# Kernel optimization log

Hardware: AMD Instinct MI355X
Metric: run time of the kernel (lower is better)

Reference implementation:

```python
import jax, jax.numpy as jnp
import numpy as np

B, L, D, H = 2, 1000, 288, 8
DIM = D // H          # 36 per-head dim
DFF = 2 * D           # 576 conv-FFN hidden
KS = L // 4           # 250 sampled keys per query
NQ = L // 4           # 250 selected (active) queries
EPS = 1e-5


def _layernorm(x, g, b):
    mu = x.mean(-1, keepdims=True)
    var = ((x - mu) ** 2).mean(-1, keepdims=True)
    return (x - mu) * jax.lax.rsqrt(var + EPS) * g + b


def _prob_attention(q, k, v, index_key):
    # q,k,v: [b,h,L,dim]; index_key: [L, KS]
    b, h, l, dim = q.shape
    # sample KS keys per query row (gather): [b,h,L,KS,dim]
    k_samp = jnp.take(k, index_key, axis=2)
    # sampled scores: [b,h,L,KS]
    scores_samp = jnp.einsum('bhld,bhlkd->bhlk', q, k_samp)
    # sparsity measure M(q) = max - mean(over full l_key, as in source)
    measure = scores_samp.max(-1) - scores_samp.sum(-1) / l
    # top-NQ active queries per (b,h): [b,h,NQ]
    idx_q = jax.lax.top_k(measure, NQ)[1]
    q_sel = jnp.take_along_axis(q, idx_q[..., None], axis=2)  # [b,h,NQ,dim]
    sim = jnp.einsum('bhqd,bhkd->bhqk', q_sel, k) * (1.0 / np.sqrt(dim))
    attn = jax.nn.softmax(sim, axis=-1)
    out_sel = jnp.einsum('bhqk,bhkd->bhqd', attn, v)          # [b,h,NQ,dim]
    # lazy queries get mean(V); scatter active outputs in
    out = jnp.broadcast_to(v.mean(axis=2, keepdims=True), v.shape)
    bi = jnp.arange(b)[:, None, None]
    hi = jnp.arange(h)[None, :, None]
    out = out.at[bi, hi, idx_q].set(out_sel)
    return out  # [b,h,L,dim]


def reference(x, index_key, Wq, bq, Wk, bk, Wv, bv, W1, b1, W2, b2,
              ln1_g, ln1_b, ln2_g, ln2_b):
    b, l, d = x.shape
    # QKV projections -> [b,h,L,dim]
    q = (x @ Wq.T + bq).reshape(b, l, H, DIM).transpose(0, 2, 1, 3)
    k = (x @ Wk.T + bk).reshape(b, l, H, DIM).transpose(0, 2, 1, 3)
    v = (x @ Wv.T + bv).reshape(b, l, H, DIM).transpose(0, 2, 1, 3)
    attn = _prob_attention(q, k, v, index_key)
    attn = attn.transpose(0, 2, 1, 3).reshape(b, l, d)
    # residual + LN1 (dropout is identity in eval)
    h1 = _layernorm(x + attn, ln1_g, ln1_b)
    # conv FFN (kernel_size=1 conv == per-position linear), exact GELU
    f = jax.nn.gelu(h1 @ W1.T + b1, approximate=False)   # [b,l,DFF]
    f = jax.nn.gelu(f @ W2.T + b2, approximate=False)    # [b,l,d]
    return _layernorm(f + h1, ln2_g, ln2_b)


def setup_inputs() -> dict:
    key = jax.random.key(0)
    ks = jax.random.split(key, 10)
    s = 0.05
    return {
        'x': jax.random.normal(ks[0], (B, L, D), jnp.float32),
        'index_key': jax.random.randint(ks[1], (L, KS), 0, L),
        'Wq': jax.random.normal(ks[2], (D, D), jnp.float32) * s,
        'bq': jnp.zeros((D,), jnp.float32),
        'Wk': jax.random.normal(ks[3], (D, D), jnp.float32) * s,
        'bk': jnp.zeros((D,), jnp.float32),
        'Wv': jax.random.normal(ks[4], (D, D), jnp.float32) * s,
        'bv': jnp.zeros((D,), jnp.float32),
        'W1': jax.random.normal(ks[5], (DFF, D), jnp.float32) * s,
        'b1': jnp.zeros((DFF,), jnp.float32),
        'W2': jax.random.normal(ks[6], (D, DFF), jnp.float32) * s,
        'b2': jnp.zeros((D,), jnp.float32),
        'ln1_g': jnp.ones((D,), jnp.float32),
        'ln1_b': jnp.zeros((D,), jnp.float32),
        'ln2_g': jnp.ones((D,), jnp.float32),
        'ln2_b': jnp.zeros((D,), jnp.float32),
    }
```

## Files before the change

kernel.cpp:

```cpp
#include <hip/hip_runtime.h>
#include <hip/hip_bf16.h>
#include <math.h>

#define B_ 2
#define L_ 1000
#define D_ 288
#define H_ 8
#define DIM_ 36
#define DFF_ 576
#define KS_ 250
#define NQ_ 250
#define BH_ (B_ * H_)
#define EPS_ 1e-5f
#define PSTRIDE_ 40

__device__ __forceinline__ float gelu_exact(float x) {
    return 0.5f * x * (1.0f + erff(x * 0.70710678118654752f));
}

__device__ __forceinline__ float dot4(float4 a, float4 b) {
    return a.x * b.x + a.y * b.y + a.z * b.z + a.w * b.w;
}

__global__ __launch_bounds__(256) void transpose_kernel(
    const float* __restrict__ src, float* __restrict__ dst,
    int Rr, int Cc, int ntx)
{
    __shared__ float tile[32][33];
    const int t = blockIdx.x;
    const int ty0 = (t / ntx) * 32, tx0 = (t % ntx) * 32;
    const int tx = threadIdx.x & 31, ty = threadIdx.x >> 5;
#pragma unroll
    for (int i = 0; i < 4; i++)
        tile[ty + 8 * i][tx] = src[(size_t)(ty0 + ty + 8 * i) * Cc + tx0 + tx];
    __syncthreads();
#pragma unroll
    for (int i = 0; i < 4; i++)
        dst[(size_t)(tx0 + ty + 8 * i) * Rr + ty0 + tx] = tile[tx][ty + 8 * i];
}

__global__ __launch_bounds__(256) void ktranspose_kernel(
    const float* __restrict__ K, float* __restrict__ KT)
{
    __shared__ float tile[32][33];
    const int t = blockIdx.x;
    const int bh = t >> 6;
    const int rem = t & 63;
    const int lt = rem >> 1, dt = rem & 1;
    const int l0 = lt * 32, d0 = dt * 32;
    const int tx = threadIdx.x & 31, ty = threadIdx.x >> 5;
    const float* Kb = K + (size_t)bh * L_ * DIM_;
    float* KTb = KT + (size_t)bh * DIM_ * L_;
#pragma unroll
    for (int i = 0; i < 4; i++) {
        int l = l0 + ty + 8 * i, d = d0 + tx;
        tile[ty + 8 * i][tx] = (l < L_ && d < DIM_) ? Kb[(size_t)l * DIM_ + d] : 0.f;
    }
    __syncthreads();
#pragma unroll
    for (int i = 0; i < 4; i++) {
        int d = d0 + ty + 8 * i, l = l0 + tx;
        if (d < DIM_ && l < L_) KTb[(size_t)d * L_ + l] = tile[tx][ty + 8 * i];
    }
}

__global__ __launch_bounds__(256) void qkvT2_kernel(
    const float* __restrict__ x,
    const float* __restrict__ WqT, const float* __restrict__ WkT,
    const float* __restrict__ WvT,
    const float* __restrict__ bq, const float* __restrict__ bk,
    const float* __restrict__ bv,
    float* __restrict__ Q, float* __restrict__ K, float* __restrict__ V)
{
    __shared__ float xsT[D_][4];
    const int base = blockIdx.x * 4;
    const int tid = threadIdx.x;

    for (int idx = tid; idx < 4 * D_; idx += 256) {
        int r = idx / D_, k = idx % D_;
        xsT[k][r] = x[(size_t)(base + r) * D_ + k];
    }
    __syncthreads();

    if (tid < 216) {
        const int gcol = 4 * tid;
        const int m = gcol / D_;
        const int c = gcol - m * D_;
        const float* WT = (m == 0) ? WqT : (m == 1) ? WkT : WvT;
        const float* bias = (m == 0) ? bq : (m == 1) ? bk : bv;
        float* outp = (m == 0) ? Q : (m == 1) ? K : V;

        float a[4][4];
#pragma unroll
        for (int j = 0; j < 4; j++) {
            float bv2 = bias[c + j];
#pragma unroll
            for (int r = 0; r < 4; r++) a[j][r] = bv2;
        }

        for (int k = 0; k < D_; k++) {
            float4 w = *(const float4*)(WT + (size_t)k * D_ + c);
            float4 xv = *(const float4*)&xsT[k][0];
            a[0][0] += w.x * xv.x; a[0][1] += w.x * xv.y; a[0][2] += w.x * xv.z; a[0][3] += w.x * xv.w;
            a[1][0] += w.y * xv.x; a[1][1] += w.y * xv.y; a[1][2] += w.y * xv.z; a[1][3] += w.y * xv.w;
            a[2][0] += w.z * xv.x; a[2][1] += w.z * xv.y; a[2][2] += w.z * xv.z; a[2][3] += w.z * xv.w;
            a[3][0] += w.w * xv.x; a[3][1] += w.w * xv.y; a[3][2] += w.w * xv.z; a[3][3] += w.w * xv.w;
        }

#pragma unroll
        for (int j = 0; j < 4; j++) {
            int col = c + j;
            int h = col / DIM_, dd = col % DIM_;
#pragma unroll
            for (int r = 0; r < 4; r++) {
                int row = base + r;
                int b = row / L_, l = row % L_;
                outp[((size_t)(b * H_ + h) * L_ + l) * DIM_ + dd] = a[j][r];
            }
        }
    }
}

__global__ __launch_bounds__(320) void qkv_kernel(
    const float* __restrict__ x,
    const float* __restrict__ Wq, const float* __restrict__ bq,
    const float* __restrict__ Wk, const float* __restrict__ bk,
    const float* __restrict__ Wv, const float* __restrict__ bv,
    float* __restrict__ Q, float* __restrict__ K, float* __restrict__ V)
{
    constexpr int R = 8;
    __shared__ float xs[R][D_];
    const int base = blockIdx.x * R;
    const int tid = threadIdx.x;

    const float4* xsrc = (const float4*)(x + (size_t)base * D_);
    float4* xdst = (float4*)&xs[0][0];
    for (int i = tid; i < R * D_ / 4; i += 320) xdst[i] = xsrc[i];
    __syncthreads();

    if (tid < D_) {
        const float4* wq4 = (const float4*)(Wq + (size_t)tid * D_);
        const float4* wk4 = (const float4*)(Wk + (size_t)tid * D_);
        const float4* wv4 = (const float4*)(Wv + (size_t)tid * D_);
        float aq[R], ak[R], av[R];
        float biasq = bq[tid], biask = bk[tid], biasv = bv[tid];
#pragma unroll
        for (int r = 0; r < R; r++) { aq[r] = biasq; ak[r] = biask; av[r] = biasv; }
        for (int d4 = 0; d4 < D_ / 4; d4++) {
            float4 wqv = wq4[d4], wkv = wk4[d4], wvv = wv4[d4];
#pragma unroll
            for (int r = 0; r < R; r++) {
                float4 hv = *(const float4*)&xs[r][d4 * 4];
                aq[r] += dot4(hv, wqv);
                ak[r] += dot4(hv, wkv);
                av[r] += dot4(hv, wvv);
            }
        }
        const int h = tid / DIM_, dd = tid % DIM_;
#pragma unroll
        for (int r = 0; r < R; r++) {
            int row = base + r;
            int b = row / L_, l = row % L_;
            size_t o = ((size_t)(b * H_ + h) * L_ + l) * DIM_ + dd;
            Q[o] = aq[r]; K[o] = ak[r]; V[o] = av[r];
        }
    }
}

__global__ __launch_bounds__(256) void vmean_kernel(
    const float* __restrict__ V, float* __restrict__ Vmean)
{
    const int bh = blockIdx.x;
    const int tid = threadIdx.x;
    __shared__ float red[7][DIM_];
    if (tid < 252) {
        int g = tid / DIM_, d = tid % DIM_;
        const float* base = V + (size_t)bh * L_ * DIM_;
        float s = 0.f;
        for (int l = g; l < L_; l += 7) s += base[l * DIM_ + d];
        red[g][d] = s;
    }
    __syncthreads();
    if (tid < DIM_) {
        float s = 0.f;
#pragma unroll
        for (int g = 0; g < 7; g++) s += red[g][tid];
        Vmean[bh * DIM_ + tid] = s * (1.0f / L_);
    }
}

__global__ __launch_bounds__(256) void score_measure3_kernel(
    const float* __restrict__ Q, const float* __restrict__ KT,
    const int* __restrict__ index_key, float* __restrict__ measure)
{
    constexpr int R = 8;
    __shared__ float qs[R][DIM_];
    __shared__ float st[R][1004];
    const int bh = blockIdx.x / 125;
    const int qt = blockIdx.x % 125;
    const int tid = threadIdx.x;

    if (tid < R * DIM_ / 4)
        ((float4*)&qs[0][0])[tid] =
            ((const float4*)(Q + ((size_t)bh * L_ + qt * R) * DIM_))[tid];
    __syncthreads();

    const float* KTb = KT + (size_t)bh * DIM_ * L_;
#pragma unroll
    for (int i = 0; i < 4; i++) {
        const int k = i * 256 + tid;
        if (k < L_) {
            float acc[R];
#pragma unroll
            for (int r = 0; r < R; r++) acc[r] = 0.f;
#pragma unroll
            for (int d4 = 0; d4 < DIM_ / 4; d4++) {
                float4 kv;
                kv.x = KTb[(size_t)(d4 * 4 + 0) * L_ + k];
                kv.y = KTb[(size_t)(d4 * 4 + 1) * L_ + k];
                kv.z = KTb[(size_t)(d4 * 4 + 2) * L_ + k];
                kv.w = KTb[(size_t)(d4 * 4 + 3) * L_ + k];
#pragma unroll
                for (int r = 0; r < R; r++)
                    acc[r] += dot4(*(const float4*)&qs[r][d4 * 4], kv);
            }
#pragma unroll
            for (int r = 0; r < R; r++) st[r][k] = acc[r];
        }
    }
    __syncthreads();

    const int r = tid >> 5;
    const int lane = tid & 31;
    const int l = qt * R + r;
    const int* ik = index_key + l * KS_;
    float mx = -1e30f, sm = 0.f;
    for (int s = lane; s < KS_; s += 32) {
        float v = st[r][ik[s]];
        mx = fmaxf(mx, v);
        sm += v;
    }
#pragma unroll
    for (int off = 16; off; off >>= 1) {
        mx = fmaxf(mx, __shfl_xor(mx, off));
        sm += __shfl_xor(sm, off);
    }
    if (lane == 0) measure[bh * L_ + l] = mx - sm * (1.0f / (float)L_);
}

__global__ __launch_bounds__(256) void measure_kernel(
    const float* __restrict__ Q, const float* __restrict__ K,
    const int* __restrict__ index_key, float* __restrict__ measure)
{
    const int w = threadIdx.x >> 6;
    const int lane = threadIdx.x & 63;
    const int wid = blockIdx.x * 4 + w;
    const int bh = wid / L_;
    const int l = wid % L_;

    const float4* qp = (const float4*)(Q + ((size_t)bh * L_ + l) * DIM_);
    float4 q[9];
#pragma unroll
    for (int i = 0; i < 9; i++) q[i] = qp[i];

    const int* ik = index_key + l * KS_;
    const float* Kb = K + (size_t)bh * L_ * DIM_;

    float mx = -1e30f, sm = 0.f;
#pragma unroll
    for (int s = lane; s < KS_; s += 64) {
        int kidx = ik[s];
        const float4* k4 = (const float4*)(Kb + (size_t)kidx * DIM_);
        float acc = 0.f;
#pragma unroll
        for (int i = 0; i < 9; i++) acc += dot4(q[i], k4[i]);
        mx = fmaxf(mx, acc);
        sm += acc;
    }
#pragma unroll
    for (int off = 32; off; off >>= 1) {
        mx = fmaxf(mx, __shfl_xor(mx, off));
        sm += __shfl_xor(sm, off);
    }
    if (lane == 0) measure[wid] = mx - sm * (1.0f / (float)L_);
}

__global__ __launch_bounds__(256) void topk_kernel(
    const float* __restrict__ measure, int* __restrict__ qlist,
    int* __restrict__ qcnt)
{
    const int bh = blockIdx.x >> 2;
    const int quarter = blockIdx.x & 3;
    __shared__ float m[L_];
    for (int i = threadIdx.x; i < L_; i += 256) m[i] = measure[bh * L_ + i];
    __syncthreads();
    const int i = quarter * 250 + threadIdx.x;
    if (threadIdx.x < 250) {
        float mi = m[i];
        int rank = 0;
        for (int j = 0; j < L_; j++) {
            float mj = m[j];
            rank += (mj > mi) || (mj == mi && j < i);
        }
        if (rank < NQ_) {
            int pos = atomicAdd(&qcnt[bh], 1);
            qlist[bh * NQ_ + pos] = i;
        }
    }
}

__global__ __launch_bounds__(256) void fill_kernel(
    const float* __restrict__ Vmean, float* __restrict__ attn_out)
{
    int idx = blockIdx.x * blockDim.x + threadIdx.x;
    if (idx >= B_ * L_ * D_) return;
    int d = idx % D_;
    int bl = idx / D_;
    int b = bl / L_;
    int h = d / DIM_, dd = d % DIM_;
    attn_out[idx] = Vmean[(b * H_ + h) * DIM_ + dd];
}

__global__ __launch_bounds__(256) void attn_part_kernel(
    const float* __restrict__ Q, const float* __restrict__ K,
    const float* __restrict__ V, const int* __restrict__ qlist,
    float* __restrict__ part, int nchunk, int chunk_len)
{
    const int bh = blockIdx.x / nchunk;
    const int chunk = blockIdx.x % nchunk;
    const int slot = threadIdx.x;
    if (slot >= NQ_) return;

    const int qidx = qlist[bh * NQ_ + slot];
    const float4* qp = (const float4*)(Q + ((size_t)bh * L_ + qidx) * DIM_);
    float4 q[9];
#pragma unroll
    for (int i = 0; i < 9; i++) q[i] = qp[i];

    const float* Kb = K + (size_t)bh * L_ * DIM_;
    const float* Vb = V + (size_t)bh * L_ * DIM_;
    const float scale = (float)(1.0 / 6.0);

    float4 acc[9];
#pragma unroll
    for (int i = 0; i < 9; i++) acc[i] = make_float4(0.f, 0.f, 0.f, 0.f);
    float sum = 0.f;

    const int k0 = chunk * chunk_len;
    for (int j = 0; j < chunk_len; j++) {
        const int key = k0 + j;
        const float4* kp = (const float4*)(Kb + (size_t)key * DIM_);
        float s = 0.f;
#pragma unroll
        for (int i = 0; i < 9; i++) s += dot4(q[i], kp[i]);
        float e = __expf(s * scale);
        sum += e;
        const float4* vp = (const float4*)(Vb + (size_t)key * DIM_);
#pragma unroll
        for (int i = 0; i < 9; i++) {
            float4 vv = vp[i];
            acc[i].x += e * vv.x;
            acc[i].y += e * vv.y;
            acc[i].z += e * vv.z;
            acc[i].w += e * vv.w;
        }
    }

    float* p = part + ((size_t)(bh * NQ_ + slot) * nchunk + chunk) * PSTRIDE_;
#pragma unroll
    for (int i = 0; i < 9; i++) ((float4*)p)[i] = acc[i];
    p[DIM_] = sum;
}

__global__ __launch_bounds__(256) void combine_kernel(
    const float* __restrict__ part, const int* __restrict__ qlist,
    float* __restrict__ attn_out, int nchunk)
{
    int idx = blockIdx.x * blockDim.x + threadIdx.x;
    if (idx >= BH_ * NQ_ * DIM_) return;
    int d = idx % DIM_;
    int bhslot = idx / DIM_;
    int bh = bhslot / NQ_, slot = bhslot % NQ_;
    const float* base = part + (size_t)bhslot * nchunk * PSTRIDE_;
    float a = 0.f, s = 0.f;
    for (int c = 0; c < nchunk; c++) {
        a += base[c * PSTRIDE_ + d];
        s += base[c * PSTRIDE_ + DIM_];
    }
    int qidx = qlist[bh * NQ_ + slot];
    int b = bh / H_, h = bh % H_;
    attn_out[((size_t)b * L_ + qidx) * D_ + h * DIM_ + d] = a / s;
}

__global__ __launch_bounds__(64) void ln1_kernel(
    const float* __restrict__ x, const float* __restrict__ attn,
    const float* __restrict__ g, const float* __restrict__ bb,
    float* __restrict__ h1)
{
    const int row = blockIdx.x;
    const int lane = threadIdx.x;
    const float* xr = x + (size_t)row * D_;
    const float* ar = attn + (size_t)row * D_;

    float vals[5];
    float s = 0.f;
#pragma unroll
    for (int i = 0; i < 5; i++) {
        int j = lane + i * 64;
        float v = (j < D_) ? (xr[j] + ar[j]) : 0.f;
        vals[i] = v;
        s += v;
    }
#pragma unroll
    for (int off = 32; off; off >>= 1) s += __shfl_xor(s, off);
    float mu = s * (1.0f / D_);

    float vs = 0.f;
#pragma unroll
    for (int i = 0; i < 5; i++) {
        int j = lane + i * 64;
        if (j < D_) { float dd = vals[i] - mu; vs += dd * dd; }
    }
#pragma unroll
    for (int off = 32; off; off >>= 1) vs += __shfl_xor(vs, off);
    float rstd = rsqrtf(vs * (1.0f / D_) + EPS_);

#pragma unroll
    for (int i = 0; i < 5; i++) {
        int j = lane + i * 64;
        if (j < D_) h1[(size_t)row * D_ + j] = (vals[i] - mu) * rstd * g[j] + bb[j];
    }
}

__global__ __launch_bounds__(288) void ffn_fused2_kernel(
    const float* __restrict__ h1,
    const float* __restrict__ W1T, const float* __restrict__ b1,
    const float* __restrict__ W2T, const float* __restrict__ b2,
    const float* __restrict__ g, const float* __restrict__ bb,
    float* __restrict__ out)
{
    __shared__ float hsT[D_][4];
    __shared__ float fsT[DFF_][4];
    __shared__ float red[3456];
    __shared__ float ys[4][D_];
    const int base = blockIdx.x * 4;
    const int tid = threadIdx.x;

    for (int idx = tid; idx < 4 * D_; idx += 288) {
        int r = idx / D_, k = idx % D_;
        hsT[k][r] = h1[(size_t)(base + r) * D_ + k];
    }
    __syncthreads();

    {
        const int kg = tid / 144;
        const int ct = tid - kg * 144;
        const int c = 4 * ct;
        float a[4][4];
        if (kg == 0) {
#pragma unroll
            for (int j = 0; j < 4; j++) {
                float bv = b1[c + j];
#pragma unroll
                for (int r = 0; r < 4; r++) a[j][r] = bv;
            }
        } else {
#pragma unroll
            for (int j = 0; j < 4; j++)
#pragma unroll
                for (int r = 0; r < 4; r++) a[j][r] = 0.f;
        }
        const int kbeg = kg * 144;
        for (int k = kbeg; k < kbeg + 144; k++) {
            float4 w = *(const float4*)(W1T + (size_t)k * DFF_ + c);
            float4 xv = *(const float4*)&hsT[k][0];
            a[0][0] += w.x * xv.x; a[0][1] += w.x * xv.y; a[0][2] += w.x * xv.z; a[0][3] += w.x * xv.w;
            a[1][0] += w.y * xv.x; a[1][1] += w.y * xv.y; a[1][2] += w.y * xv.z; a[1][3] += w.y * xv.w;
            a[2][0] += w.z * xv.x; a[2][1] += w.z * xv.y; a[2][2] += w.z * xv.z; a[2][3] += w.z * xv.w;
            a[3][0] += w.w * xv.x; a[3][1] += w.w * xv.y; a[3][2] += w.w * xv.z; a[3][3] += w.w * xv.w;
        }
        if (kg == 1) {
#pragma unroll
            for (int j = 0; j < 4; j++)
#pragma unroll
                for (int r = 0; r < 4; r++) red[ct * 16 + j * 4 + r] = a[j][r];
        }
        __syncthreads();
        if (kg == 0) {
#pragma unroll
            for (int j = 0; j < 4; j++)
#pragma unroll
                for (int r = 0; r < 4; r++)
                    fsT[c + j][r] = gelu_exact(a[j][r] + red[ct * 16 + j * 4 + r]);
        }
    }
    __syncthreads();

    {
        const int kg = tid / 72;
        const int ct = tid - kg * 72;
        const int c = 4 * ct;
        float a[4][4];
        if (kg == 0) {
#pragma unroll
            for (int j = 0; j < 4; j++) {
                float bv = b2[c + j];
#pragma unroll
                for (int r = 0; r < 4; r++) a[j][r] = bv;
            }
        } else {
#pragma unroll
            for (int j = 0; j < 4; j++)
#pragma unroll
                for (int r = 0; r < 4; r++) a[j][r] = 0.f;
        }
        const int kbeg = kg * 144;
        for (int k = kbeg; k < kbeg + 144; k++) {
            float4 w = *(const float4*)(W2T + (size_t)k * D_ + c);
            float4 fv = *(const float4*)&fsT[k][0];
            a[0][0] += w.x * fv.x; a[0][1] += w.x * fv.y; a[0][2] += w.x * fv.z; a[0][3] += w.x * fv.w;
            a[1][0] += w.y * fv.x; a[1][1] += w.y * fv.y; a[1][2] += w.y * fv.z; a[1][3] += w.y * fv.w;
            a[2][0] += w.z * fv.x; a[2][1] += w.z * fv.y; a[2][2] += w.z * fv.z; a[2][3] += w.z * fv.w;
            a[3][0] += w.w * fv.x; a[3][1] += w.w * fv.y; a[3][2] += w.w * fv.z; a[3][3] += w.w * fv.w;
        }
        if (kg >= 1) {
#pragma unroll
            for (int j = 0; j < 4; j++)
#pragma unroll
                for (int r = 0; r < 4; r++)
                    red[((kg - 1) * 72 + ct) * 16 + j * 4 + r] = a[j][r];
        }
        __syncthreads();
        if (kg == 0) {
#pragma unroll
            for (int j = 0; j < 4; j++)
#pragma unroll
                for (int r = 0; r < 4; r++) {
                    float v = a[j][r];
                    v += red[(0 * 72 + ct) * 16 + j * 4 + r];
                    v += red[(1 * 72 + ct) * 16 + j * 4 + r];
                    v += red[(2 * 72 + ct) * 16 + j * 4 + r];
                    ys[r][c + j] = gelu_exact(v) + hsT[c + j][r];
                }
        }
    }
    __syncthreads();

    const int w = tid >> 6;
    const int lane = tid & 63;
    if (w < 4) {
        const int r = w;
        float s = 0.f, ss = 0.f;
#pragma unroll
        for (int i = 0; i < 5; i++) {
            int j = lane + i * 64;
            if (j < D_) { float y = ys[r][j]; s += y; ss += y * y; }
        }
#pragma unroll
        for (int off = 32; off; off >>= 1) {
            s += __shfl_xor(s, off);
            ss += __shfl_xor(ss, off);
        }
        float mu = s * (1.0f / D_);
        float var = ss * (1.0f / D_) - mu * mu;
        float rstd = rsqrtf(var + EPS_);
        int row = base + r;
#pragma unroll
        for (int i = 0; i < 5; i++) {
            int j = lane + i * 64;
            if (j < D_) out[(size_t)row * D_ + j] = (ys[r][j] - mu) * rstd * g[j] + bb[j];
        }
    }
}

__global__ __launch_bounds__(192) void ffn1_kernel(
    const float* __restrict__ h1,
    const float* __restrict__ W1, const float* __restrict__ b1,
    float* __restrict__ f1)
{
    constexpr int R = 8;
    __shared__ float hs[R][D_];
    const int base = blockIdx.x * R;
    const int tid = threadIdx.x;

    const float4* hsrc = (const float4*)(h1 + (size_t)base * D_);
    float4* hdst = (float4*)&hs[0][0];
    for (int i = tid; i < R * D_ / 4; i += 192) hdst[i] = hsrc[i];
    __syncthreads();

    const int j0 = tid, j1 = tid + 192, j2 = tid + 384;
    const float4* w0 = (const float4*)(W1 + (size_t)j0 * D_);
    const float4* w1 = (const float4*)(W1 + (size_t)j1 * D_);
    const float4* w2 = (const float4*)(W1 + (size_t)j2 * D_);
    float a0[R], a1[R], a2[R];
    float bb0 = b1[j0], bb1 = b1[j1], bb2 = b1[j2];
#pragma unroll
    for (int r = 0; r < R; r++) { a0[r] = bb0; a1[r] = bb1; a2[r] = bb2; }

    for (int d4 = 0; d4 < D_ / 4; d4++) {
        float4 x0 = w0[d4], x1 = w1[d4], x2 = w2[d4];
#pragma unroll
        for (int r = 0; r < R; r++) {
            float4 hv = *(const float4*)&hs[r][d4 * 4];
            a0[r] += dot4(hv, x0);
            a1[r] += dot4(hv, x1);
            a2[r] += dot4(hv, x2);
        }
    }
#pragma unroll
    for (int r = 0; r < R; r++) {
        size_t rowo = (size_t)(base + r) * DFF_;
        f1[rowo + j0] = gelu_exact(a0[r]);
        f1[rowo + j1] = gelu_exact(a1[r]);
        f1[rowo + j2] = gelu_exact(a2[r]);
    }
}

__global__ __launch_bounds__(320) void ffn2_ln_kernel(
    const float* __restrict__ f1, const float* __restrict__ h1,
    const float* __restrict__ W2, const float* __restrict__ b2,
    const float* __restrict__ g, const float* __restrict__ bb,
    float* __restrict__ out)
{
    constexpr int R = 8;
    __shared__ float fs[R][DFF_];
    __shared__ float hs[R][D_];
    __shared__ float ys[R][D_];
    const int base = blockIdx.x * R;
    const int tid = threadIdx.x;

    const float4* fsrc = (const float4*)(f1 + (size_t)base * DFF_);
    float4* fdst = (float4*)&fs[0][0];
    for (int i = tid; i < R * DFF_ / 4; i += 320) fdst[i] = fsrc[i];
    const float4* hsrc = (const float4*)(h1 + (size_t)base * D_);
    float4* hdst = (float4*)&hs[0][0];
    for (int i = tid; i < R * D_ / 4; i += 320) hdst[i] = hsrc[i];
    __syncthreads();

    if (tid < D_) {
        const float4* w4 = (const float4*)(W2 + (size_t)tid * DFF_);
        float acc[R];
        float bias = b2[tid];
#pragma unroll
        for (int r = 0; r < R; r++) acc[r] = bias;
        for (int d4 = 0; d4 < DFF_ / 4; d4++) {
            float4 wv = w4[d4];
#pragma unroll
            for (int r = 0; r < R; r++) {
                float4 fv = *(const float4*)&fs[r][d4 * 4];
                acc[r] += dot4(fv, wv);
            }
        }
#pragma unroll
        for (int r = 0; r < R; r++) ys[r][tid] = gelu_exact(acc[r]) + hs[r][tid];
    }
    __syncthreads();

    const int w = tid >> 6;
    const int lane = tid & 63;
    for (int r = w; r < R; r += 5) {
        float s = 0.f, ss = 0.f;
#pragma unroll
        for (int i = 0; i < 5; i++) {
            int j = lane + i * 64;
            if (j < D_) { float y = ys[r][j]; s += y; ss += y * y; }
        }
#pragma unroll
        for (int off = 32; off; off >>= 1) {
            s += __shfl_xor(s, off);
            ss += __shfl_xor(ss, off);
        }
        float mu = s * (1.0f / D_);
        float var = ss * (1.0f / D_) - mu * mu;
        float rstd = rsqrtf(var + EPS_);
        int row = base + r;
#pragma unroll
        for (int i = 0; i < 5; i++) {
            int j = lane + i * 64;
            if (j < D_) out[(size_t)row * D_ + j] = (ys[r][j] - mu) * rstd * g[j] + bb[j];
        }
    }
}

extern "C" void kernel_launch(void* const* d_in, const int* in_sizes, int n_in,
                              void* d_out, int out_size, void* d_ws, size_t ws_size,
                              hipStream_t stream)
{
    const float* x         = (const float*)d_in[0];
    const int*   index_key = (const int*)  d_in[1];
    const float* Wq = (const float*)d_in[2];
    const float* bq = (const float*)d_in[3];
    const float* Wk = (const float*)d_in[4];
    const float* bk = (const float*)d_in[5];
    const float* Wv = (const float*)d_in[6];
    const float* bv = (const float*)d_in[7];
    const float* W1 = (const float*)d_in[8];
    const float* b1 = (const float*)d_in[9];
    const float* W2 = (const float*)d_in[10];
    const float* b2 = (const float*)d_in[11];
    const float* ln1_g = (const float*)d_in[12];
    const float* ln1_b = (const float*)d_in[13];
    const float* ln2_g = (const float*)d_in[14];
    const float* ln2_b = (const float*)d_in[15];
    float* out = (float*)d_out;

    float* Q        = (float*)d_ws;
    float* K        = Q + 576000;
    float* V        = K + 576000;
    float* Vmean    = V + 576000;
    float* measure  = Vmean + 576;
    float* attn_out = measure + 16000;
    float* h1       = attn_out + 576000;
    int*   qlist    = (int*)(h1 + 576000);
    int*   qcnt     = qlist + 4000;
    float* part     = (float*)(qcnt + 16);
    float* f1       = part;
    float* KT       = part + 4000000;

    float* WqT = part;
    float* WkT = WqT + 82944;
    float* WvT = WkT + 82944;
    float* W1T = part;
    float* W2T = part + 165888;

    const size_t kt_end = 2900592ull + 4000000ull + 576000ull;
    const bool   big    = ws_size >= kt_end * sizeof(float);
    const int    nchunk = big ? 25 : 8;
    const int    chunk_len = L_ / nchunk;

    if (big) {
        transpose_kernel<<<81, 256, 0, stream>>>(Wq, WqT, D_, D_, 9);
        transpose_kernel<<<81, 256, 0, stream>>>(Wk, WkT, D_, D_, 9);
        transpose_kernel<<<81, 256, 0, stream>>>(Wv, WvT, D_, D_, 9);
        qkvT2_kernel<<<500, 256, 0, stream>>>(x, WqT, WkT, WvT, bq, bk, bv, Q, K, V);
    } else {
        qkv_kernel<<<250, 320, 0, stream>>>(x, Wq, bq, Wk, bk, Wv, bv, Q, K, V);
    }
    vmean_kernel<<<BH_, 256, 0, stream>>>(V, Vmean);
    if (big) {
        ktranspose_kernel<<<BH_ * 64, 256, 0, stream>>>(K, KT);
        score_measure3_kernel<<<BH_ * 125, 256, 0, stream>>>(Q, KT, index_key, measure);
    } else {
        measure_kernel<<<4000, 256, 0, stream>>>(Q, K, index_key, measure);
    }
    hipMemsetAsync(qcnt, 0, BH_ * sizeof(int), stream);
    topk_kernel<<<BH_ * 4, 256, 0, stream>>>(measure, qlist, qcnt);
    fill_kernel<<<(B_ * L_ * D_ + 255) / 256, 256, 0, stream>>>(Vmean, attn_out);
    attn_part_kernel<<<BH_ * nchunk, 256, 0, stream>>>(Q, K, V, qlist, part, nchunk, chunk_len);
    combine_kernel<<<(BH_ * NQ_ * DIM_ + 255) / 256, 256, 0, stream>>>(part, qlist, attn_out, nchunk);
    ln1_kernel<<<B_ * L_, 64, 0, stream>>>(x, attn_out, ln1_g, ln1_b, h1);
    if (big) {
        transpose_kernel<<<162, 256, 0, stream>>>(W1, W1T, DFF_, D_, 9);
        transpose_kernel<<<162, 256, 0, stream>>>(W2, W2T, D_, DFF_, 18);
        ffn_fused2_kernel<<<500, 288, 0, stream>>>(h1, W1T, b1, W2T, b2, ln2_g, ln2_b, out);
    } else {
        ffn1_kernel<<<250, 192, 0, stream>>>(h1, W1, b1, f1);
        ffn2_ln_kernel<<<250, 320, 0, stream>>>(f1, h1, W2, b2, ln2_g, ln2_b, out);
    }
}
```

Before: 315.4 us.

## Fuse lazy-fill, partial combine and LN1 via slot map; merge QKV weight transposes

Topk now records, for each query position, its slot in the active-query list, with -1 marking lazy queries. A new finalize_ln1 kernel uses that map to read either the V mean or the combined attention partials per element, adds the residual and applies LayerNorm1 in one pass. This replaces the fill, combine and ln1 kernels and no longer writes or reads the attn_out buffer. It adds one memset and scattered reads of partials inside the LayerNorm kernel. Separately, the three QKV weight transposes are merged into one launch.

```diff
diff --git a/kernel.cpp b/kernel.cpp
--- a/kernel.cpp
+++ b/kernel.cpp
@@ -39,6 +39,27 @@
         dst[(size_t)(tx0 + ty + 8 * i) * Rr + ty0 + tx] = tile[tx][ty + 8 * i];
 }
 
+__global__ __launch_bounds__(256) void qkv_transpose_kernel(
+    const float* __restrict__ Wq, const float* __restrict__ Wk,
+    const float* __restrict__ Wv,
+    float* __restrict__ WqT, float* __restrict__ WkT, float* __restrict__ WvT)
+{
+    __shared__ float tile[32][33];
+    const int m = blockIdx.x / 81;
+    const int t = blockIdx.x % 81;
+    const float* src = (m == 0) ? Wq : (m == 1) ? Wk : Wv;
+    float* dst = (m == 0) ? WqT : (m == 1) ? WkT : WvT;
+    const int ty0 = (t / 9) * 32, tx0 = (t % 9) * 32;
+    const int tx = threadIdx.x & 31, ty = threadIdx.x >> 5;
+#pragma unroll
+    for (int i = 0; i < 4; i++)
+        tile[ty + 8 * i][tx] = src[(size_t)(ty0 + ty + 8 * i) * D_ + tx0 + tx];
+    __syncthreads();
+#pragma unroll
+    for (int i = 0; i < 4; i++)
+        dst[(size_t)(tx0 + ty + 8 * i) * D_ + ty0 + tx] = tile[tx][ty + 8 * i];
+}
+
 __global__ __launch_bounds__(256) void ktranspose_kernel(
     const float* __restrict__ K, float* __restrict__ KT)
 {
@@ -287,7 +308,7 @@
 
 __global__ __launch_bounds__(256) void topk_kernel(
     const float* __restrict__ measure, int* __restrict__ qlist,
-    int* __restrict__ qcnt)
+    int* __restrict__ qcnt, int* __restrict__ slot_map)
 {
     const int bh = blockIdx.x >> 2;
     const int quarter = blockIdx.x & 3;
@@ -305,6 +326,7 @@
         if (rank < NQ_) {
             int pos = atomicAdd(&qcnt[bh], 1);
             qlist[bh * NQ_ + pos] = i;
+            slot_map[bh * L_ + i] = pos;
         }
     }
 }
@@ -390,6 +412,63 @@
     int qidx = qlist[bh * NQ_ + slot];
     int b = bh / H_, h = bh % H_;
     attn_out[((size_t)b * L_ + qidx) * D_ + h * DIM_ + d] = a / s;
+}
+
+__global__ __launch_bounds__(64) void finalize_ln1_kernel(
+    const float* __restrict__ part, const int* __restrict__ slot_map,
+    const float* __restrict__ Vmean, const float* __restrict__ x,
+    const float* __restrict__ g, const float* __restrict__ bb,
+    float* __restrict__ h1, int nchunk)
+{
+    const int row = blockIdx.x;
+    const int b = row / L_, l = row % L_;
+    const int lane = threadIdx.x;
+
+    float vals[5];
+    float s = 0.f;
+#pragma unroll
+    for (int i = 0; i < 5; i++) {
+        int j = lane + i * 64;
+        float v = 0.f;
+        if (j < D_) {
+            int h = j / DIM_, dd = j - h * DIM_;
+            int bh = b * H_ + h;
+            int slot = slot_map[bh * L_ + l];
+            if (slot < 0) {
+                v = Vmean[bh * DIM_ + dd];
+            } else {
+                const float* p = part + (size_t)(bh * NQ_ + slot) * nchunk * PSTRIDE_;
+                float a = 0.f, ssum = 0.f;
+                for (int c = 0; c < nchunk; c++) {
+                    a += p[c * PSTRIDE_ + dd];
+                    ssum += p[c * PSTRIDE_ + DIM_];
+                }
+                v = a / ssum;
+            }
+            v += x[(size_t)row * D_ + j];
+        }
+        vals[i] = v;
+        s += v;
+    }
+#pragma unroll
+    for (int off = 32; off; off >>= 1) s += __shfl_xor(s, off);
+    float mu = s * (1.0f / D_);
+
+    float vs = 0.f;
+#pragma unroll
+    for (int i = 0; i < 5; i++) {
+        int j = lane + i * 64;
+        if (j < D_) { float dd = vals[i] - mu; vs += dd * dd; }
+    }
+#pragma unroll
+    for (int off = 32; off; off >>= 1) vs += __shfl_xor(vs, off);
+    float rstd = rsqrtf(vs * (1.0f / D_) + EPS_);
+
+#pragma unroll
+    for (int i = 0; i < 5; i++) {
+        int j = lane + i * 64;
+        if (j < D_) h1[(size_t)row * D_ + j] = (vals[i] - mu) * rstd * g[j] + bb[j];
+    }
 }
 
 __global__ __launch_bounds__(64) void ln1_kernel(
@@ -713,7 +792,8 @@
     float* h1       = attn_out + 576000;
     int*   qlist    = (int*)(h1 + 576000);
     int*   qcnt     = qlist + 4000;
-    float* part     = (float*)(qcnt + 16);
+    int*   slot_map = qcnt + 16;
+    float* part     = (float*)(slot_map + 16000);
     float* f1       = part;
     float* KT       = part + 4000000;
 
@@ -723,15 +803,13 @@
     float* W1T = part;
     float* W2T = part + 165888;
 
-    const size_t kt_end = 2900592ull + 4000000ull + 576000ull;
+    const size_t kt_end = 2916608ull + 4000000ull + 576000ull;
     const bool   big    = ws_size >= kt_end * sizeof(float);
     const int    nchunk = big ? 25 : 8;
     const int    chunk_len = L_ / nchunk;
 
     if (big) {
-        transpose_kernel<<<81, 256, 0, stream>>>(Wq, WqT, D_, D_, 9);
-        transpose_kernel<<<81, 256, 0, stream>>>(Wk, WkT, D_, D_, 9);
-        transpose_kernel<<<81, 256, 0, stream>>>(Wv, WvT, D_, D_, 9);
+        qkv_transpose_kernel<<<243, 256, 0, stream>>>(Wq, Wk, Wv, WqT, WkT, WvT);
         qkvT2_kernel<<<500, 256, 0, stream>>>(x, WqT, WkT, WvT, bq, bk, bv, Q, K, V);
     } else {
         qkv_kernel<<<250, 320, 0, stream>>>(x, Wq, bq, Wk, bk, Wv, bv, Q, K, V);
@@ -744,11 +822,11 @@
         measure_kernel<<<4000, 256, 0, stream>>>(Q, K, index_key, measure);
     }
     hipMemsetAsync(qcnt, 0, BH_ * sizeof(int), stream);
-    topk_kernel<<<BH_ * 4, 256, 0, stream>>>(measure, qlist, qcnt);
-    fill_kernel<<<(B_ * L_ * D_ + 255) / 256, 256, 0, stream>>>(Vmean, attn_out);
+    hipMemsetAsync(slot_map, 0xFF, BH_ * L_ * sizeof(int), stream);
+    topk_kernel<<<BH_ * 4, 256, 0, stream>>>(measure, qlist, qcnt, slot_map);
     attn_part_kernel<<<BH_ * nchunk, 256, 0, stream>>>(Q, K, V, qlist, part, nchunk, chunk_len);
-    combine_kernel<<<(BH_ * NQ_ * DIM_ + 255) / 256, 256, 0, stream>>>(part, qlist, attn_out, nchunk);
-    ln1_kernel<<<B_ * L_, 64, 0, stream>>>(x, attn_out, ln1_g, ln1_b, h1);
+    finalize_ln1_kernel<<<B_ * L_, 64, 0, stream>>>(part, slot_map, Vmean, x,
+                                                    ln1_g, ln1_b, h1, nchunk);
     if (big) {
         transpose_kernel<<<162, 256, 0, stream>>>(W1, W1T, DFF_, D_, 9);
         transpose_kernel<<<162, 256, 0, stream>>>(W2, W2T, D_, DFF_, 18);
```

After: 329.8 us. 4.6% more time.
